# Kernel optimization log

Measured on AMD Instinct MI355X. Metric: run time of the kernel, lower is better.

Reference implementation:

```python
import jax, jax.numpy as jnp
import numpy as np

D_MODEL = 1024
N_HEADS = 16
D_KEY = 64
ALIBI_SLOPE = 8.0
B, S = 2, 2048


def setup_inputs() -> dict:
    key = jax.random.key(0)
    ks = jax.random.split(key, 10)
    sd = D_MODEL ** -0.5
    states = jax.random.normal(ks[0], (B, S, D_MODEL), dtype=jnp.float32)
    bias_mask = jax.random.normal(ks[1], (B, S, S), dtype=jnp.float32)
    # non-trainable ALiBi-style per-head scale
    head_scale = jnp.exp2(-((jnp.arange(N_HEADS, dtype=jnp.float32) + 1.0) * ALIBI_SLOPE / N_HEADS))
    # parameters (torch Linear: y = x @ W.T + b)
    Wa = jax.random.normal(ks[2], (N_HEADS, D_MODEL), dtype=jnp.float32) * sd  # a_proj, no bias
    Wv = jax.random.normal(ks[3], (D_MODEL, D_MODEL), dtype=jnp.float32) * sd
    bv = jnp.zeros((D_MODEL,), dtype=jnp.float32)
    Wg = jax.random.normal(ks[4], (N_HEADS, D_MODEL), dtype=jnp.float32) * sd
    bg = jnp.zeros((N_HEADS,), dtype=jnp.float32)
    Wo = jax.random.normal(ks[5], (D_MODEL, D_MODEL), dtype=jnp.float32) * sd
    bo = jnp.zeros((D_MODEL,), dtype=jnp.float32)
    return {"states": states, "bias_mask": bias_mask, "head_scale": head_scale,
            "Wa": Wa, "Wv": Wv, "bv": bv, "Wg": Wg, "bg": bg, "Wo": Wo, "bo": bo}


def reference(states, bias_mask, head_scale, Wa, Wv, bv, Wg, bg, Wo, bo):
    # bias: [B,1,Q,K] * [1,H,1,1] -> [B,H,Q,K]
    bias = bias_mask[:, None, :, :] * head_scale[None, :, None, None]
    # values: [B,K,H,dk]
    v = (jnp.einsum('bkm,dm->bkd', states, Wv) + bv).reshape(states.shape[0], states.shape[1], N_HEADS, D_KEY)
    # key-only scores: [B,S,H] -> [B,H,1,K], plus bias -> [B,H,Q,K]
    a = jnp.einsum('bkm,hm->bhk', states, Wa)[:, :, None, :] + bias
    a = jax.nn.softmax(a, axis=-1)
    o = jnp.einsum('bhqk,bkhd->bqhd', a, v)
    g = jnp.einsum('bqm,hm->bqh', states, Wg) + bg
    o = o * jax.nn.sigmoid(g)[..., None]
    o = o.reshape(o.shape[0], o.shape[1], D_MODEL)
    return jnp.einsum('bqm,dm->bqd', o, Wo) + bo
```

## Files before the change

### kernel.cpp

```cpp
#include <hip/hip_runtime.h>


#define LOG2E 1.44269504088896f

using f16   = _Float16;
using f16x4 = __attribute__((ext_vector_type(4))) _Float16;
using f16x8 = __attribute__((ext_vector_type(8))) _Float16;
using f32x4 = __attribute__((ext_vector_type(4))) float;

#define GLDS16(g, l) __builtin_amdgcn_global_load_lds((const __attribute__((address_space(1))) void*)(g), (__attribute__((address_space(3))) void*)(l), 16, 0, 0)

__global__ __launch_bounds__(256) void k_prep(
    const float* __restrict__ states, const float* __restrict__ mask,
    const float* __restrict__ Wa, const float* __restrict__ Wv,
    const float* __restrict__ Wg, const float* __restrict__ Wo,
    f16* __restrict__ st16, f16* __restrict__ Wv16, f16* __restrict__ Wo16,
    f16* __restrict__ Wag16, float* __restrict__ partial)
{
  __shared__ float ws4[4];
  const int bid = blockIdx.x;
  const int t   = threadIdx.x;
  if (bid < 1024) {
    const int row = bid * 4 + (t >> 6);
    const int lane = t & 63;
    const float* sp = states + (size_t)row * 1024 + lane * 16;
    float4 v0 = ((const float4*)sp)[0];
    float4 v1 = ((const float4*)sp)[1];
    float4 v2 = ((const float4*)sp)[2];
    float4 v3 = ((const float4*)sp)[3];
    f16x8 h0, h1;
    h0[0]=(f16)v0.x; h0[1]=(f16)v0.y; h0[2]=(f16)v0.z; h0[3]=(f16)v0.w;
    h0[4]=(f16)v1.x; h0[5]=(f16)v1.y; h0[6]=(f16)v1.z; h0[7]=(f16)v1.w;
    h1[0]=(f16)v2.x; h1[1]=(f16)v2.y; h1[2]=(f16)v2.z; h1[3]=(f16)v2.w;
    h1[4]=(f16)v3.x; h1[5]=(f16)v3.y; h1[6]=(f16)v3.z; h1[7]=(f16)v3.w;
    f16* dp = st16 + (size_t)row * 1024 + lane * 16;
    *(f16x8*)dp = h0; *(f16x8*)(dp + 8) = h1;
  } else {
    const int cb = bid - 1024;
    {
      int idx = cb * 2048 + t * 8;
      const float* src; f16* dst;
      if (idx < 1048576)      { src = Wv + idx;             dst = Wv16 + idx; }
      else if (idx < 2097152) { src = Wo + (idx - 1048576); dst = Wo16 + (idx - 1048576); }
      else { int j = idx - 2097152;
             src = (j < 16384) ? (Wa + j) : (Wg + (j - 16384));
             dst = Wag16 + j; }
      float4 v0 = ((const float4*)src)[0];
      float4 v1 = ((const float4*)src)[1];
      f16x8 h;
      h[0]=(f16)v0.x; h[1]=(f16)v0.y; h[2]=(f16)v0.z; h[3]=(f16)v0.w;
      h[4]=(f16)v1.x; h[5]=(f16)v1.y; h[6]=(f16)v1.z; h[7]=(f16)v1.w;
      *(f16x8*)dst = h;
    }
    if (cb < 512) {
      const float4* mp = (const float4*)(mask + (size_t)cb * 16384);
      float mx = 0.f;
      for (int i = 0; i < 16; ++i) {
        float4 v = mp[t + i * 256];
        mx = fmaxf(mx, fmaxf(fmaxf(fabsf(v.x), fabsf(v.y)), fmaxf(fabsf(v.z), fabsf(v.w))));
      }
      #pragma unroll
      for (int off = 32; off; off >>= 1) mx = fmaxf(mx, __shfl_xor(mx, off, 64));
      if ((t & 63) == 0) ws4[t >> 6] = mx;
      __syncthreads();
      if (t == 0) partial[cb] = fmaxf(fmaxf(ws4[0], ws4[1]), fmaxf(ws4[2], ws4[3]));
    }
  }
}

__global__ __launch_bounds__(256) void k_sg(
    const f16* __restrict__ A, const f16* __restrict__ Bw,
    const float* __restrict__ bg,
    f16* __restrict__ s16, float* __restrict__ gsig, float* __restrict__ partialS)
{
  __shared__ f16 As[2 * 4096], Bs[2 * 1024];
  const int bi = blockIdx.x;
  const int r0 = bi * 128;
  const int b  = bi >> 4;
  const int t = threadIdx.x, wid = t >> 6, lane = t & 63;
  const int lane15 = lane & 15, lg = lane >> 4;
  const int wm = wid >> 1, wn = wid & 1;
  f32x4 acc[4] = {};
  const int sswz = ((t & 3) ^ ((t >> 3) & 3)) * 8;
  const f16* ga0 = A  + (size_t)(r0 + (t >> 2)) * 1024      + sswz;
  const f16* ga1 = A  + (size_t)(r0 + 64 + (t >> 2)) * 1024 + sswz;
  const f16* gb0 = Bw + (size_t)(t >> 2) * 1024             + sswz;
  int ra[4], rb;
  #pragma unroll
  for (int m = 0; m < 4; ++m) { int r_ = wm*64 + m*16 + lane15; ra[m] = r_*32 + ((lg ^ ((r_>>1)&3)) * 8); }
  { int r_ = wn*16 + lane15; rb = r_*32 + ((lg ^ ((r_>>1)&3)) * 8); }

  #define STAGE_SG(kt, bb) do { const int k0_ = (kt) * 32; \
      GLDS16(ga0 + k0_, As + (bb)*4096 + wid*512); \
      GLDS16(ga1 + k0_, As + (bb)*4096 + 2048 + wid*512); \
      if (wid < 2) GLDS16(gb0 + k0_, Bs + (bb)*1024 + wid*512); } while(0)
  STAGE_SG(0, 0);
  for (int kt = 0; kt < 32; ++kt) {
    const int cur = kt & 1;
    if (kt < 31) {
      STAGE_SG(kt + 1, cur ^ 1);
      if (wid < 2) asm volatile("s_waitcnt vmcnt(3)" ::: "memory");
      else         asm volatile("s_waitcnt vmcnt(2)" ::: "memory");
    } else {
      asm volatile("s_waitcnt vmcnt(0)" ::: "memory");
    }
    __builtin_amdgcn_s_barrier();
    f16x8 a[4], bf;
    #pragma unroll
    for (int m = 0; m < 4; ++m) a[m] = *(const f16x8*)(As + cur*4096 + ra[m]);
    bf = *(const f16x8*)(Bs + cur*1024 + rb);
    #pragma unroll
    for (int m = 0; m < 4; ++m)
      acc[m] = __builtin_amdgcn_mfma_f32_16x16x32_f16(a[m], bf, acc[m], 0, 0, 0);
    asm volatile("s_waitcnt lgkmcnt(0)" ::: "memory");
    __builtin_amdgcn_s_barrier();
  }
  #undef STAGE_SG
  const int c = wn * 16 + lane15;
  if (wn == 0) {
    float mx = -1e30f;
    #pragma unroll
    for (int m = 0; m < 4; ++m) {
      const int q0 = (r0 & 2047) + wm * 64 + m * 16 + lg * 4;
      f16x4 hv;
      #pragma unroll
      for (int r = 0; r < 4; ++r) { mx = fmaxf(mx, acc[m][r]); hv[r] = (f16)acc[m][r]; }
      *(f16x4*)(s16 + (size_t)(b * 16 + c) * 2048 + q0) = hv;
    }
    mx = fmaxf(mx, __shfl_xor(mx, 16, 64));
    mx = fmaxf(mx, __shfl_xor(mx, 32, 64));
    if (lg == 0) partialS[(bi * 2 + wm) * 16 + c] = mx;
  } else {
    const float bgv = bg[c - 16];
    #pragma unroll
    for (int m = 0; m < 4; ++m) {
      const int q0 = (r0 & 2047) + wm * 64 + m * 16 + lg * 4;
      #pragma unroll
      for (int r = 0; r < 4; ++r) {
        const float g = acc[m][r] + bgv;
        gsig[(size_t)(b * 2048 + q0 + r) * 16 + (c - 16)] = 1.f / (1.f + __expf(-g));
      }
    }
  }
}

__global__ __launch_bounds__(64) void k_lmax(
    const float* __restrict__ partialS, const float* __restrict__ partial,
    const float* __restrict__ hs, float* __restrict__ Lbuf)
{
  const int bh = blockIdx.x, l = threadIdx.x;
  const int b = bh >> 4, h = bh & 15;
  float mx = -1e30f;
  if (l < 32) mx = partialS[((b * 16 + (l >> 1)) * 2 + (l & 1)) * 16 + h];
  float mm = 0.f;
  for (int i = l; i < 256; i += 64) mm = fmaxf(mm, partial[b * 256 + i]);
  #pragma unroll
  for (int off = 32; off; off >>= 1) {
    mx = fmaxf(mx, __shfl_xor(mx, off, 64));
    mm = fmaxf(mm, __shfl_xor(mm, off, 64));
  }
  if (l == 0) Lbuf[bh] = mx + hs[h] * mm;
}

__global__ __launch_bounds__(256) void k_gemm_v(
    const f16* __restrict__ A, const f16* __restrict__ Bw,
    const float* __restrict__ bv, f16* __restrict__ vt)
{
  __shared__ f16 As[2 * 4096], Bs[2 * 2048];
  const int p = blockIdx.x;
  const int l = (p & 7) * 64 + (p >> 3);
  const int r0 = (l >> 4) * 128, n0 = (l & 15) * 64;
  const int t = threadIdx.x, wid = t >> 6, lane = t & 63;
  const int lane15 = lane & 15, lg = lane >> 4;
  const int wr = wid >> 1, wc = wid & 1;
  f32x4 acc[4][2] = {};
  const int sswz = ((t & 3) ^ ((t >> 3) & 3)) * 8;
  const f16* ga0 = A  + (size_t)(r0 + (t >> 2)) * 1024       + sswz;
  const f16* ga1 = A  + (size_t)(r0 + 64 + (t >> 2)) * 1024  + sswz;
  const f16* gb0 = Bw + (size_t)(n0 + (t >> 2)) * 1024       + sswz;
  int ra[4], rb[2];
  #pragma unroll
  for (int m = 0; m < 4; ++m) { int r_ = wr*64 + m*16 + lane15; ra[m] = r_*32 + ((lg ^ ((r_>>1)&3)) * 8); }
  #pragma unroll
  for (int n = 0; n < 2; ++n) { int r_ = wc*32 + n*16 + lane15; rb[n] = r_*32 + ((lg ^ ((r_>>1)&3)) * 8); }

  #define STAGE_G(kt, bb) do { const int k0_ = (kt) * 32; \
      GLDS16(ga0 + k0_, As + (bb)*4096 + wid*512); \
      GLDS16(ga1 + k0_, As + (bb)*4096 + 2048 + wid*512); \
      GLDS16(gb0 + k0_, Bs + (bb)*2048 + wid*512); } while(0)
  STAGE_G(0, 0);
  for (int kt = 0; kt < 32; ++kt) {
    const int cur = kt & 1;
    if (kt < 31) {
      STAGE_G(kt + 1, cur ^ 1);
      asm volatile("s_waitcnt vmcnt(3)" ::: "memory");
    } else {
      asm volatile("s_waitcnt vmcnt(0)" ::: "memory");
    }
    __builtin_amdgcn_s_barrier();
    f16x8 a[4], bf[2];
    #pragma unroll
    for (int m = 0; m < 4; ++m) a[m] = *(const f16x8*)(As + cur*4096 + ra[m]);
    #pragma unroll
    for (int n = 0; n < 2; ++n) bf[n] = *(const f16x8*)(Bs + cur*2048 + rb[n]);
    #pragma unroll
    for (int m = 0; m < 4; ++m)
      #pragma unroll
      for (int n = 0; n < 2; ++n)
        acc[m][n] = __builtin_amdgcn_mfma_f32_16x16x32_f16(a[m], bf[n], acc[m][n], 0, 0, 0);
    asm volatile("s_waitcnt lgkmcnt(0)" ::: "memory");
    __builtin_amdgcn_s_barrier();
  }
  #undef STAGE_G
  const int b_ = r0 >> 11;
  #pragma unroll
  for (int n = 0; n < 2; ++n) {
    const int gn = n0 + wc * 32 + n * 16 + lane15;
    const float bvv = bv[gn];
    #pragma unroll
    for (int m = 0; m < 4; ++m) {
      const int kb = (r0 & 2047) + wr * 64 + m * 16 + lg * 4;
      f16x4 hv;
      #pragma unroll
      for (int r = 0; r < 4; ++r) hv[r] = (f16)(acc[m][n][r] + bvv);
      *(f16x4*)(vt + (size_t)(b_ * 1024 + gn) * 2048 + kb) = hv;
    }
  }
}

__global__ __launch_bounds__(256, 4) void k_attn(
    const float* __restrict__ mask, const f16* __restrict__ s16,
    const float* __restrict__ gsig, const float* __restrict__ hs,
    const float* __restrict__ Lbuf, const f16* __restrict__ vt,
    f16* __restrict__ og)
{
  __shared__ __align__(16) f16 mks[2 * 4096];
  __shared__ __align__(16) f16 vs[2 * 4096];

  const int p = blockIdx.x;
  const int l = (p & 7) * 128 + (p >> 3);
  const int b = l >> 9, rr = l & 511;
  const int qt = rr >> 4, h = rr & 15;

  const int t = threadIdx.x, wid = t >> 6, lane = t & 63;
  const int lane15 = lane & 15, lg = lane >> 4;
  const float L   = Lbuf[b * 16 + h];
  const float c2  = hs[h] * LOG2E;
  const float nLc = -L * LOG2E;

  const f16* vtb = vt + (size_t)(b * 1024 + h * 64) * 2048;
  const int q16 = wid * 16 + lane15;

  const int mrow = t >> 2;
  const float* msrc = mask + (size_t)b * 4194304 + (size_t)(qt * 64 + mrow) * 2048 + (t & 3) * 16;
  const f16* sptr = s16 + (size_t)(b * 16 + h) * 2048 + lg * 8;

  const int mw0 = mrow * 64 + ((((t & 3) * 2    ) ^ (mrow & 7)) * 8);
  const int mw1 = mrow * 64 + ((((t & 3) * 2 + 1) ^ (mrow & 7)) * 8);
  const int mr0 = q16 * 64 + (((    lg) ^ (q16 & 7)) * 8);
  const int mr1 = q16 * 64 + (((4 + lg) ^ (q16 & 7)) * 8);

  const int vswz = ((t & 7) ^ ((t >> 3) & 7)) * 8;
  const f16* vsrc0 = vtb + (size_t)(     (t >> 3)) * 2048 + vswz;
  const f16* vsrc1 = vtb + (size_t)(32 + (t >> 3)) * 2048 + vswz;
  int voff[2][4];
  #pragma unroll
  for (int kk = 0; kk < 2; ++kk)
    #pragma unroll
    for (int n = 0; n < 4; ++n)
      voff[kk][n] = (n * 16 + lane15) * 64 + (((kk * 4 + lg) ^ (lane15 & 7)) * 8);

  f32x4 acc[4] = {};
  float den = 0.f;
  f32x4 mg0, mg1, mg2, mg3;

  #define MLOAD(KV) do { \
    mg0 = *(const f32x4*)(msrc + (KV));      mg1 = *(const f32x4*)(msrc + (KV) + 4); \
    mg2 = *(const f32x4*)(msrc + (KV) + 8);  mg3 = *(const f32x4*)(msrc + (KV) + 12); } while (0)

  #define MWRITE(BB) do { \
    f16x8 h0_, h1_; \
    h0_[0]=(f16)mg0[0]; h0_[1]=(f16)mg0[1]; h0_[2]=(f16)mg0[2]; h0_[3]=(f16)mg0[3]; \
    h0_[4]=(f16)mg1[0]; h0_[5]=(f16)mg1[1]; h0_[6]=(f16)mg1[2]; h0_[7]=(f16)mg1[3]; \
    h1_[0]=(f16)mg2[0]; h1_[1]=(f16)mg2[1]; h1_[2]=(f16)mg2[2]; h1_[3]=(f16)mg2[3]; \
    h1_[4]=(f16)mg3[0]; h1_[5]=(f16)mg3[1]; h1_[6]=(f16)mg3[2]; h1_[7]=(f16)mg3[3]; \
    *(f16x8*)(mks + (BB)*4096 + mw0) = h0_; \
    *(f16x8*)(mks + (BB)*4096 + mw1) = h1_; } while (0)

  #define STAGE_V(KV, BB) do { \
    GLDS16(vsrc0 + (KV), vs + (BB)*4096 +        wid*512); \
    GLDS16(vsrc1 + (KV), vs + (BB)*4096 + 2048 + wid*512); } while (0)

  #define KKBODY(KK, SH, CUR) do { \
    f16x8 mh = *(const f16x8*)(mks + (CUR)*4096 + ((KK) ? mr1 : mr0)); \
    f16x8 vf0 = *(const f16x8*)(vs + (CUR)*4096 + voff[KK][0]); \
    f16x8 vf1 = *(const f16x8*)(vs + (CUR)*4096 + voff[KK][1]); \
    f16x8 vf2 = *(const f16x8*)(vs + (CUR)*4096 + voff[KK][2]); \
    f16x8 vf3 = *(const f16x8*)(vs + (CUR)*4096 + voff[KK][3]); \
    f16x8 af; float dl_ = 0.f; \
    _Pragma("unroll") \
    for (int j_ = 0; j_ < 8; ++j_) { \
      float sxj = fmaf((float)SH[j_], LOG2E, nLc); \
      float w_ = __builtin_amdgcn_exp2f(fmaf(c2, (float)mh[j_], sxj)); \
      dl_ += w_; af[j_] = (f16)w_; \
    } \
    den += dl_; \
    acc[0] = __builtin_amdgcn_mfma_f32_16x16x32_f16(af, vf0, acc[0], 0, 0, 0); \
    acc[1] = __builtin_amdgcn_mfma_f32_16x16x32_f16(af, vf1, acc[1], 0, 0, 0); \
    acc[2] = __builtin_amdgcn_mfma_f32_16x16x32_f16(af, vf2, acc[2], 0, 0, 0); \
    acc[3] = __builtin_amdgcn_mfma_f32_16x16x32_f16(af, vf3, acc[3], 0, 0, 0); } while (0)

  MLOAD(0);
  STAGE_V(0, 0);
  asm volatile("s_waitcnt vmcnt(2)" ::: "memory");
  MWRITE(0);
  asm volatile("s_waitcnt lgkmcnt(0)" ::: "memory");

  #pragma unroll 1
  for (int kt = 0; kt < 32; ++kt) {
    const int kv = kt * 64;
    const int cur = kt & 1;
    f16x8 s0r = *(const f16x8*)(sptr + kv);
    f16x8 s1r = *(const f16x8*)(sptr + kv + 32);
    if (kt < 31) {
      MLOAD(kv + 64);
      STAGE_V(kv + 64, cur ^ 1);
      asm volatile("s_waitcnt vmcnt(8)" ::: "memory");
    } else {
      asm volatile("s_waitcnt vmcnt(2)" ::: "memory");
    }
    __builtin_amdgcn_s_barrier();
    KKBODY(0, s0r, cur);
    KKBODY(1, s1r, cur);
    if (kt < 31) {
      asm volatile("s_waitcnt vmcnt(2)" ::: "memory");
      MWRITE(cur ^ 1);
    }
    asm volatile("s_waitcnt lgkmcnt(0)" ::: "memory");
    __builtin_amdgcn_s_barrier();
  }
  #undef KKBODY
  #undef STAGE_V
  #undef MWRITE
  #undef MLOAD

  den += __shfl_xor(den, 16, 64);
  den += __shfl_xor(den, 32, 64);

  #pragma unroll
  for (int r = 0; r < 4; ++r) {
    const int ql = lg * 4 + r;
    const int q = qt * 64 + wid * 16 + ql;
    const float dq = __shfl(den, ql, 64);
    const float sc = gsig[(size_t)(b * 2048 + q) * 16 + h] / dq;
    #pragma unroll
    for (int n = 0; n < 4; ++n)
      og[(size_t)(b * 2048 + q) * 1024 + h * 64 + n * 16 + lane15] = (f16)(acc[n][r] * sc);
  }
}

__global__ __launch_bounds__(256) void k_gemm_out(
    const f16* __restrict__ A, const f16* __restrict__ Bw,
    const float* __restrict__ bo, float* __restrict__ out)
{
  __shared__ f16 As[2 * 4096], Bs[2 * 2048];
  const int p = blockIdx.x;
  const int l = (p & 7) * 64 + (p >> 3);
  const int r0 = (l >> 4) * 128, n0 = (l & 15) * 64;
  const int t = threadIdx.x, wid = t >> 6, lane = t & 63;
  const int lane15 = lane & 15, lg = lane >> 4;
  const int wr = wid >> 1, wc = wid & 1;
  f32x4 acc[4][2] = {};
  const int sswz = ((t & 3) ^ ((t >> 3) & 3)) * 8;
  const f16* ga0 = A  + (size_t)(r0 + (t >> 2)) * 1024       + sswz;
  const f16* ga1 = A  + (size_t)(r0 + 64 + (t >> 2)) * 1024  + sswz;
  const f16* gb0 = Bw + (size_t)(n0 + (t >> 2)) * 1024       + sswz;
  int ra[4], rb[2];
  #pragma unroll
  for (int m = 0; m < 4; ++m) { int r_ = wr*64 + m*16 + lane15; ra[m] = r_*32 + ((lg ^ ((r_>>1)&3)) * 8); }
  #pragma unroll
  for (int n = 0; n < 2; ++n) { int r_ = wc*32 + n*16 + lane15; rb[n] = r_*32 + ((lg ^ ((r_>>1)&3)) * 8); }

  #define STAGE_G(kt, bb) do { const int k0_ = (kt) * 32; \
      GLDS16(ga0 + k0_, As + (bb)*4096 + wid*512); \
      GLDS16(ga1 + k0_, As + (bb)*4096 + 2048 + wid*512); \
      GLDS16(gb0 + k0_, Bs + (bb)*2048 + wid*512); } while(0)
  STAGE_G(0, 0);
  for (int kt = 0; kt < 32; ++kt) {
    const int cur = kt & 1;
    if (kt < 31) {
      STAGE_G(kt + 1, cur ^ 1);
      asm volatile("s_waitcnt vmcnt(3)" ::: "memory");
    } else {
      asm volatile("s_waitcnt vmcnt(0)" ::: "memory");
    }
    __builtin_amdgcn_s_barrier();
    f16x8 a[4], bf[2];
    #pragma unroll
    for (int m = 0; m < 4; ++m) a[m] = *(const f16x8*)(As + cur*4096 + ra[m]);
    #pragma unroll
    for (int n = 0; n < 2; ++n) bf[n] = *(const f16x8*)(Bs + cur*2048 + rb[n]);
    #pragma unroll
    for (int m = 0; m < 4; ++m)
      #pragma unroll
      for (int n = 0; n < 2; ++n)
        acc[m][n] = __builtin_amdgcn_mfma_f32_16x16x32_f16(a[m], bf[n], acc[m][n], 0, 0, 0);
    asm volatile("s_waitcnt lgkmcnt(0)" ::: "memory");
    __builtin_amdgcn_s_barrier();
  }
  #undef STAGE_G
  #pragma unroll
  for (int n = 0; n < 2; ++n) {
    const int gn = n0 + wc * 32 + n * 16 + lane15;
    const float bov = bo[gn];
    #pragma unroll
    for (int m = 0; m < 4; ++m) {
      const int rbase = r0 + wr * 64 + m * 16 + lg * 4;
      #pragma unroll
      for (int r = 0; r < 4; ++r)
        out[(size_t)(rbase + r) * 1024 + gn] = acc[m][n][r] + bov;
    }
  }
}

extern "C" void kernel_launch(void* const* d_in, const int* in_sizes, int n_in,
                              void* d_out, int out_size, void* d_ws, size_t ws_size,
                              hipStream_t stream)
{
  const float* states = (const float*)d_in[0];
  const float* mask   = (const float*)d_in[1];
  const float* hs     = (const float*)d_in[2];
  const float* Wa     = (const float*)d_in[3];
  const float* Wv     = (const float*)d_in[4];
  const float* bv     = (const float*)d_in[5];
  const float* Wg     = (const float*)d_in[6];
  const float* bg     = (const float*)d_in[7];
  const float* Wo     = (const float*)d_in[8];
  const float* bo     = (const float*)d_in[9];
  float* out = (float*)d_out;

  char* ws = (char*)d_ws;
  f16*   st16     = (f16*)(ws);
  f16*   og       = (f16*)(ws);
  f16*   Wv16     = (f16*)(ws + 8388608);
  f16*   Wo16     = (f16*)(ws + 10485760);
  f16*   Wag16    = (f16*)(ws + 12582912);
  float* gsig     = (float*)(ws + 12648448);
  f16*   s16      = (f16*)(ws + 12910592);
  float* partial  = (float*)(ws + 13041664);
  float* partialS = (float*)(ws + 13043712);
  float* Lbuf     = (float*)(ws + 13047808);
  f16*   vt       = (f16*)(ws + 13107200);

  k_prep<<<2064, 256, 0, stream>>>(states, mask, Wa, Wv, Wg, Wo,
                                   st16, Wv16, Wo16, Wag16, partial);
  k_sg<<<32, 256, 0, stream>>>(st16, Wag16, bg, s16, gsig, partialS);
  k_lmax<<<32, 64, 0, stream>>>(partialS, partial, hs, Lbuf);
  k_gemm_v<<<512, 256, 0, stream>>>(st16, Wv16, bv, vt);
  k_attn<<<1024, 256, 0, stream>>>(mask, s16, gsig, hs, Lbuf, vt, og);
  k_gemm_out<<<512, 256, 0, stream>>>(og, Wo16, bo, out);
}
```

Baseline: 133.3 us.

## Use 32x32 MFMA with 128-query attention tiles and precomputed fp32 key scores

The attention kernel now processes 128 query rows per block instead of 64 and uses 32x32x16 MFMA instructions, so each V tile staged in LDS serves twice as many queries and fewer, larger matrix ops are issued. The per-key score term (s*log2e - L*log2e) is precomputed in fp32 in k_lmax, which removes a conversion and FMA from the inner loop. In exchange the attention kernel uses more LDS and registers (occupancy hint lowered to 2), launches half as many blocks, and reads the key scores as fp32, which doubles that traffic.

```diff
diff --git a/kernel.cpp b/kernel.cpp
--- a/kernel.cpp
+++ b/kernel.cpp
@@ -7,6 +7,7 @@
 using f16x4 = __attribute__((ext_vector_type(4))) _Float16;
 using f16x8 = __attribute__((ext_vector_type(8))) _Float16;
 using f32x4 = __attribute__((ext_vector_type(4))) float;
+using f32x16 = __attribute__((ext_vector_type(16))) float;
 
 #define GLDS16(g, l) __builtin_amdgcn_global_load_lds((const __attribute__((address_space(1))) void*)(g), (__attribute__((address_space(3))) void*)(l), 16, 0, 0)
 
@@ -146,7 +147,8 @@
 
 __global__ __launch_bounds__(64) void k_lmax(
     const float* __restrict__ partialS, const float* __restrict__ partial,
-    const float* __restrict__ hs, float* __restrict__ Lbuf)
+    const float* __restrict__ hs, const f16* __restrict__ s16,
+    float* __restrict__ s32L)
 {
   const int bh = blockIdx.x, l = threadIdx.x;
   const int b = bh >> 4, h = bh & 15;
@@ -159,7 +161,11 @@
     mx = fmaxf(mx, __shfl_xor(mx, off, 64));
     mm = fmaxf(mm, __shfl_xor(mm, off, 64));
   }
-  if (l == 0) Lbuf[bh] = mx + hs[h] * mm;
+  const float nL = -(mx + hs[h] * mm) * LOG2E;
+  for (int j = 0; j < 32; ++j) {
+    const int i = j * 64 + l;
+    s32L[(size_t)bh * 2048 + i] = fmaf((float)s16[(size_t)bh * 2048 + i], LOG2E, nL);
+  }
 }
 
 __global__ __launch_bounds__(256) void k_gemm_v(
@@ -228,87 +234,104 @@
   }
 }
 
-__global__ __launch_bounds__(256, 4) void k_attn(
-    const float* __restrict__ mask, const f16* __restrict__ s16,
+__global__ __launch_bounds__(256, 2) void k_attn(
+    const float* __restrict__ mask, const float* __restrict__ s32L,
     const float* __restrict__ gsig, const float* __restrict__ hs,
-    const float* __restrict__ Lbuf, const f16* __restrict__ vt,
-    f16* __restrict__ og)
-{
-  __shared__ __align__(16) f16 mks[2 * 4096];
+    const f16* __restrict__ vt, f16* __restrict__ og)
+{
+  __shared__ __align__(16) f16 mks[2 * 8192];
   __shared__ __align__(16) f16 vs[2 * 4096];
 
   const int p = blockIdx.x;
-  const int l = (p & 7) * 128 + (p >> 3);
-  const int b = l >> 9, rr = l & 511;
+  const int l = (p & 7) * 64 + (p >> 3);
+  const int b = l >> 8, rr = l & 255;
   const int qt = rr >> 4, h = rr & 15;
 
   const int t = threadIdx.x, wid = t >> 6, lane = t & 63;
-  const int lane15 = lane & 15, lg = lane >> 4;
-  const float L   = Lbuf[b * 16 + h];
-  const float c2  = hs[h] * LOG2E;
-  const float nLc = -L * LOG2E;
+  const int l31 = lane & 31, l5 = lane >> 5;
+  const float c2 = hs[h] * LOG2E;
+
+  const int mrow = t >> 1, mhalf = t & 1;
+  const float* msrc = mask + (size_t)b * 4194304 + (size_t)(qt * 128 + mrow) * 2048 + mhalf * 32;
+  int mwoff[4];
+  #pragma unroll
+  for (int u = 0; u < 4; ++u)
+    mwoff[u] = mrow * 64 + (((mhalf * 4 + u) ^ (mrow & 7)) * 8);
+
+  const int qrow = wid * 32 + l31;
+  int moff[4];
+  #pragma unroll
+  for (int ks = 0; ks < 4; ++ks)
+    moff[ks] = qrow * 64 + (((l5 + 2 * ks) ^ (qrow & 7)) * 8);
+
+  const float* sptr = s32L + (size_t)(b * 16 + h) * 2048 + l5 * 8;
 
   const f16* vtb = vt + (size_t)(b * 1024 + h * 64) * 2048;
-  const int q16 = wid * 16 + lane15;
-
-  const int mrow = t >> 2;
-  const float* msrc = mask + (size_t)b * 4194304 + (size_t)(qt * 64 + mrow) * 2048 + (t & 3) * 16;
-  const f16* sptr = s16 + (size_t)(b * 16 + h) * 2048 + lg * 8;
-
-  const int mw0 = mrow * 64 + ((((t & 3) * 2    ) ^ (mrow & 7)) * 8);
-  const int mw1 = mrow * 64 + ((((t & 3) * 2 + 1) ^ (mrow & 7)) * 8);
-  const int mr0 = q16 * 64 + (((    lg) ^ (q16 & 7)) * 8);
-  const int mr1 = q16 * 64 + (((4 + lg) ^ (q16 & 7)) * 8);
-
   const int vswz = ((t & 7) ^ ((t >> 3) & 7)) * 8;
   const f16* vsrc0 = vtb + (size_t)(     (t >> 3)) * 2048 + vswz;
   const f16* vsrc1 = vtb + (size_t)(32 + (t >> 3)) * 2048 + vswz;
-  int voff[2][4];
-  #pragma unroll
-  for (int kk = 0; kk < 2; ++kk)
-    #pragma unroll
-    for (int n = 0; n < 4; ++n)
-      voff[kk][n] = (n * 16 + lane15) * 64 + (((kk * 4 + lg) ^ (lane15 & 7)) * 8);
-
-  f32x4 acc[4] = {};
+  int voffA[4], voffB[4];
+  #pragma unroll
+  for (int ks = 0; ks < 4; ++ks) {
+    voffA[ks] = (     l31) * 64 + (((2 * ks + l5) ^ (l31 & 7)) * 8);
+    voffB[ks] = (32 + l31) * 64 + (((2 * ks + l5) ^ (l31 & 7)) * 8);
+  }
+
+  f32x16 acc0 = {}, acc1 = {};
   float den = 0.f;
-  f32x4 mg0, mg1, mg2, mg3;
+  f32x4 mg0, mg1, mg2, mg3, mg4, mg5, mg6, mg7;
+  f32x4 sv0, sv1, sv2, sv3, sv4, sv5, sv6, sv7;
 
   #define MLOAD(KV) do { \
-    mg0 = *(const f32x4*)(msrc + (KV));      mg1 = *(const f32x4*)(msrc + (KV) + 4); \
-    mg2 = *(const f32x4*)(msrc + (KV) + 8);  mg3 = *(const f32x4*)(msrc + (KV) + 12); } while (0)
+    mg0 = *(const f32x4*)(msrc + (KV));      mg1 = *(const f32x4*)(msrc + (KV) + 4);  \
+    mg2 = *(const f32x4*)(msrc + (KV) + 8);  mg3 = *(const f32x4*)(msrc + (KV) + 12); \
+    mg4 = *(const f32x4*)(msrc + (KV) + 16); mg5 = *(const f32x4*)(msrc + (KV) + 20); \
+    mg6 = *(const f32x4*)(msrc + (KV) + 24); mg7 = *(const f32x4*)(msrc + (KV) + 28); } while (0)
 
   #define MWRITE(BB) do { \
-    f16x8 h0_, h1_; \
+    f16x8 h0_, h1_, h2_, h3_; \
     h0_[0]=(f16)mg0[0]; h0_[1]=(f16)mg0[1]; h0_[2]=(f16)mg0[2]; h0_[3]=(f16)mg0[3]; \
     h0_[4]=(f16)mg1[0]; h0_[5]=(f16)mg1[1]; h0_[6]=(f16)mg1[2]; h0_[7]=(f16)mg1[3]; \
     h1_[0]=(f16)mg2[0]; h1_[1]=(f16)mg2[1]; h1_[2]=(f16)mg2[2]; h1_[3]=(f16)mg2[3]; \
     h1_[4]=(f16)mg3[0]; h1_[5]=(f16)mg3[1]; h1_[6]=(f16)mg3[2]; h1_[7]=(f16)mg3[3]; \
-    *(f16x8*)(mks + (BB)*4096 + mw0) = h0_; \
-    *(f16x8*)(mks + (BB)*4096 + mw1) = h1_; } while (0)
+    h2_[0]=(f16)mg4[0]; h2_[1]=(f16)mg4[1]; h2_[2]=(f16)mg4[2]; h2_[3]=(f16)mg4[3]; \
+    h2_[4]=(f16)mg5[0]; h2_[5]=(f16)mg5[1]; h2_[6]=(f16)mg5[2]; h2_[7]=(f16)mg5[3]; \
+    h3_[0]=(f16)mg6[0]; h3_[1]=(f16)mg6[1]; h3_[2]=(f16)mg6[2]; h3_[3]=(f16)mg6[3]; \
+    h3_[4]=(f16)mg7[0]; h3_[5]=(f16)mg7[1]; h3_[6]=(f16)mg7[2]; h3_[7]=(f16)mg7[3]; \
+    *(f16x8*)(mks + (BB)*8192 + mwoff[0]) = h0_; \
+    *(f16x8*)(mks + (BB)*8192 + mwoff[1]) = h1_; \
+    *(f16x8*)(mks + (BB)*8192 + mwoff[2]) = h2_; \
+    *(f16x8*)(mks + (BB)*8192 + mwoff[3]) = h3_; } while (0)
+
+  #define SLOAD(KV) do { \
+    sv0 = *(const f32x4*)(sptr + (KV));      sv1 = *(const f32x4*)(sptr + (KV) + 4);  \
+    sv2 = *(const f32x4*)(sptr + (KV) + 16); sv3 = *(const f32x4*)(sptr + (KV) + 20); \
+    sv4 = *(const f32x4*)(sptr + (KV) + 32); sv5 = *(const f32x4*)(sptr + (KV) + 36); \
+    sv6 = *(const f32x4*)(sptr + (KV) + 48); sv7 = *(const f32x4*)(sptr + (KV) + 52); } while (0)
 
   #define STAGE_V(KV, BB) do { \
     GLDS16(vsrc0 + (KV), vs + (BB)*4096 +        wid*512); \
     GLDS16(vsrc1 + (KV), vs + (BB)*4096 + 2048 + wid*512); } while (0)
 
-  #define KKBODY(KK, SH, CUR) do { \
-    f16x8 mh = *(const f16x8*)(mks + (CUR)*4096 + ((KK) ? mr1 : mr0)); \
-    f16x8 vf0 = *(const f16x8*)(vs + (CUR)*4096 + voff[KK][0]); \
-    f16x8 vf1 = *(const f16x8*)(vs + (CUR)*4096 + voff[KK][1]); \
-    f16x8 vf2 = *(const f16x8*)(vs + (CUR)*4096 + voff[KK][2]); \
-    f16x8 vf3 = *(const f16x8*)(vs + (CUR)*4096 + voff[KK][3]); \
+  #define KSBODY(KS, SA, SB, CUR) do { \
+    f16x8 mh  = *(const f16x8*)(mks + (CUR)*8192 + moff[KS]); \
+    f16x8 vfA = *(const f16x8*)(vs + (CUR)*4096 + voffA[KS]); \
+    f16x8 vfB = *(const f16x8*)(vs + (CUR)*4096 + voffB[KS]); \
     f16x8 af; float dl_ = 0.f; \
-    _Pragma("unroll") \
-    for (int j_ = 0; j_ < 8; ++j_) { \
-      float sxj = fmaf((float)SH[j_], LOG2E, nLc); \
-      float w_ = __builtin_amdgcn_exp2f(fmaf(c2, (float)mh[j_], sxj)); \
-      dl_ += w_; af[j_] = (f16)w_; \
-    } \
+    float w0 = __builtin_amdgcn_exp2f(fmaf(c2, (float)mh[0], SA[0])); \
+    float w1 = __builtin_amdgcn_exp2f(fmaf(c2, (float)mh[1], SA[1])); \
+    float w2 = __builtin_amdgcn_exp2f(fmaf(c2, (float)mh[2], SA[2])); \
+    float w3 = __builtin_amdgcn_exp2f(fmaf(c2, (float)mh[3], SA[3])); \
+    float w4 = __builtin_amdgcn_exp2f(fmaf(c2, (float)mh[4], SB[0])); \
+    float w5 = __builtin_amdgcn_exp2f(fmaf(c2, (float)mh[5], SB[1])); \
+    float w6 = __builtin_amdgcn_exp2f(fmaf(c2, (float)mh[6], SB[2])); \
+    float w7 = __builtin_amdgcn_exp2f(fmaf(c2, (float)mh[7], SB[3])); \
+    af[0]=(f16)w0; af[1]=(f16)w1; af[2]=(f16)w2; af[3]=(f16)w3; \
+    af[4]=(f16)w4; af[5]=(f16)w5; af[6]=(f16)w6; af[7]=(f16)w7; \
+    dl_ = ((w0 + w1) + (w2 + w3)) + ((w4 + w5) + (w6 + w7)); \
     den += dl_; \
-    acc[0] = __builtin_amdgcn_mfma_f32_16x16x32_f16(af, vf0, acc[0], 0, 0, 0); \
-    acc[1] = __builtin_amdgcn_mfma_f32_16x16x32_f16(af, vf1, acc[1], 0, 0, 0); \
-    acc[2] = __builtin_amdgcn_mfma_f32_16x16x32_f16(af, vf2, acc[2], 0, 0, 0); \
-    acc[3] = __builtin_amdgcn_mfma_f32_16x16x32_f16(af, vf3, acc[3], 0, 0, 0); } while (0)
+    acc0 = __builtin_amdgcn_mfma_f32_32x32x16_f16(af, vfA, acc0, 0, 0, 0); \
+    acc1 = __builtin_amdgcn_mfma_f32_32x32x16_f16(af, vfB, acc1, 0, 0, 0); } while (0)
 
   MLOAD(0);
   STAGE_V(0, 0);
@@ -320,18 +343,19 @@
   for (int kt = 0; kt < 32; ++kt) {
     const int kv = kt * 64;
     const int cur = kt & 1;
-    f16x8 s0r = *(const f16x8*)(sptr + kv);
-    f16x8 s1r = *(const f16x8*)(sptr + kv + 32);
+    SLOAD(kv);
     if (kt < 31) {
       MLOAD(kv + 64);
       STAGE_V(kv + 64, cur ^ 1);
+      asm volatile("s_waitcnt vmcnt(18)" ::: "memory");
+    } else {
       asm volatile("s_waitcnt vmcnt(8)" ::: "memory");
-    } else {
-      asm volatile("s_waitcnt vmcnt(2)" ::: "memory");
-    }
-    __builtin_amdgcn_s_barrier();
-    KKBODY(0, s0r, cur);
-    KKBODY(1, s1r, cur);
+    }
+    __builtin_amdgcn_s_barrier();
+    KSBODY(0, sv0, sv1, cur);
+    KSBODY(1, sv2, sv3, cur);
+    KSBODY(2, sv4, sv5, cur);
+    KSBODY(3, sv6, sv7, cur);
     if (kt < 31) {
       asm volatile("s_waitcnt vmcnt(2)" ::: "memory");
       MWRITE(cur ^ 1);
@@ -339,23 +363,23 @@
     asm volatile("s_waitcnt lgkmcnt(0)" ::: "memory");
     __builtin_amdgcn_s_barrier();
   }
-  #undef KKBODY
+  #undef KSBODY
   #undef STAGE_V
+  #undef SLOAD
   #undef MWRITE
   #undef MLOAD
 
-  den += __shfl_xor(den, 16, 64);
   den += __shfl_xor(den, 32, 64);
 
-  #pragma unroll
-  for (int r = 0; r < 4; ++r) {
-    const int ql = lg * 4 + r;
-    const int q = qt * 64 + wid * 16 + ql;
+  const int qb4 = l5 * 4;
+  #pragma unroll
+  for (int r = 0; r < 16; ++r) {
+    const int ql = (r & 3) + 8 * (r >> 2) + qb4;
+    const int qg = qt * 128 + wid * 32 + ql;
     const float dq = __shfl(den, ql, 64);
-    const float sc = gsig[(size_t)(b * 2048 + q) * 16 + h] / dq;
-    #pragma unroll
-    for (int n = 0; n < 4; ++n)
-      og[(size_t)(b * 2048 + q) * 1024 + h * 64 + n * 16 + lane15] = (f16)(acc[n][r] * sc);
+    const float sc = gsig[(size_t)(b * 2048 + qg) * 16 + h] / dq;
+    og[(size_t)(b * 2048 + qg) * 1024 + h * 64 +      l31] = (f16)(acc0[r] * sc);
+    og[(size_t)(b * 2048 + qg) * 1024 + h * 64 + 32 + l31] = (f16)(acc1[r] * sc);
   }
 }
 
@@ -449,14 +473,14 @@
   f16*   s16      = (f16*)(ws + 12910592);
   float* partial  = (float*)(ws + 13041664);
   float* partialS = (float*)(ws + 13043712);
-  float* Lbuf     = (float*)(ws + 13047808);
   f16*   vt       = (f16*)(ws + 13107200);
+  float* s32L     = (float*)(ws + 21495808);
 
   k_prep<<<2064, 256, 0, stream>>>(states, mask, Wa, Wv, Wg, Wo,
                                    st16, Wv16, Wo16, Wag16, partial);
   k_sg<<<32, 256, 0, stream>>>(st16, Wag16, bg, s16, gsig, partialS);
-  k_lmax<<<32, 64, 0, stream>>>(partialS, partial, hs, Lbuf);
+  k_lmax<<<32, 64, 0, stream>>>(partialS, partial, hs, s16, s32L);
   k_gemm_v<<<512, 256, 0, stream>>>(st16, Wv16, bv, vt);
-  k_attn<<<1024, 256, 0, stream>>>(mask, s16, gsig, hs, Lbuf, vt, og);
+  k_attn<<<512, 256, 0, stream>>>(mask, s32L, gsig, hs, vt, og);
   k_gemm_out<<<512, 256, 0, stream>>>(og, Wo16, bo, out);
 }
```

After: 166.4 us. 24.8% more time.
